# Kernel tuning notes

Hardware: AMD Instinct MI355X
Metric: run time of the kernel (lower is better)

The kernel has to match this reference:

```python
import jax, jax.numpy as jnp
import numpy as np

B, T, N, D, M, H, L, FF = 8, 128, 24, 128, 9, 8, 4, 1024
F = D // H          # spatial head dim = 16
HD = D // H         # temporal head dim = 16
ND = N * D          # 3072
NM = N * M          # 216


def setup_inputs() -> dict:
    key = jax.random.key(0)
    ks = jax.random.split(key, 24)
    w = lambda k, shape, s=0.05: (jax.random.normal(k, shape, jnp.float32) * s)
    z = lambda shape: jnp.zeros(shape, jnp.float32)
    return {
        "inputs": jax.random.normal(ks[0], (B, T, NM), jnp.float32),
        "emb_W": w(ks[1], (N, M, D)), "emb_b": z((N, D)),
        "sp_Wq": w(ks[2], (L, H, N, D, F)), "sp_bq": z((L, H, N, F)),
        "sp_Wk": w(ks[3], (L, H, D, F)), "sp_bk": z((L, H, F)),
        "sp_Wv": w(ks[4], (L, H, D, F)), "sp_bv": z((L, H, F)),
        "tmp_Win": w(ks[5], (L, N, 3 * D, D)), "tmp_bin": z((L, N, 3 * D)),
        "tmp_Wout": w(ks[6], (L, N, D, D)), "tmp_bout": z((L, N, D)),
        "ff_W1": w(ks[7], (L, ND, FF)), "ff_b1": z((L, FF)),
        "ff_W2": w(ks[8], (L, FF, ND)), "ff_b2": z((L, ND)),
        "ln_g": jnp.ones((L, ND), jnp.float32), "ln_b": z((L, ND)),
        "fin_W": w(ks[9], (ND, NM)), "fin_b": z((NM,)),
    }


def _ln(x, g, b):
    m = jnp.mean(x, -1, keepdims=True)
    v = jnp.mean(jnp.square(x - m), -1, keepdims=True)
    return (x - m) * jax.lax.rsqrt(v + 1e-5) * g + b


def _pos_encoding():
    # standard sinusoidal PE; original adds it over the FIRST axis of the
    # (B, T, N*D) tensor (applied before the permute), so index by B.
    pos = jnp.arange(B, dtype=jnp.float32)[:, None]
    div = jnp.exp(jnp.arange(0, ND, 2, dtype=jnp.float32) * (-np.log(10000.0) / ND))
    pe = jnp.zeros((B, ND), jnp.float32)
    pe = pe.at[:, 0::2].set(jnp.sin(pos * div)).at[:, 1::2].set(jnp.cos(pos * div))
    return pe


def reference(inputs, emb_W, emb_b, sp_Wq, sp_bq, sp_Wk, sp_bk, sp_Wv, sp_bv,
              tmp_Win, tmp_bin, tmp_Wout, tmp_bout, ff_W1, ff_b1, ff_W2, ff_b2,
              ln_g, ln_b, fin_W, fin_b):
    # joint embedding: (B,T,N,M) @ (N,M,D) -> (B,T,N,D)
    x4 = inputs.reshape(B, T, N, M)
    emb = (jnp.einsum('btnm,nmd->btnd', x4, emb_W) + emb_b).reshape(B, T, ND)
    emb = emb + _pos_encoding()[:, None, :]
    h = emb.transpose(1, 0, 2)                     # (T, B, ND)
    # PyTorch float attn_mask is ADDED to scores: +1.0 strictly below diagonal
    mask = jnp.tril(jnp.ones((T, T), jnp.float32), -1)
    for l in range(L):
        xr = h.reshape(T, B, N, D)
        # ---- spatial attention (shared K/V, per-joint Q, per head) ----
        k = jnp.einsum('tbnd,hdf->tbhnf', xr, sp_Wk[l]) + sp_bk[l][:, None, :]
        v = jnp.einsum('tbnd,hdf->tbhnf', xr, sp_Wv[l]) + sp_bv[l][:, None, :]
        q = jnp.einsum('tbnd,hndf->tbhnf', xr, sp_Wq[l]) + sp_bq[l]
        a = jax.nn.softmax(jnp.einsum('tbhnf,tbhmf->tbhnm', q, k) / jnp.sqrt(jnp.float32(F)), -1)
        sp = jnp.einsum('tbhnm,tbhmf->tbhnf', a, v)
        sp = sp.transpose(0, 1, 3, 2, 4).reshape(T, B, ND)   # joint-major, heads concat within joint
        sp = _ln(sp + h, ln_g[l], ln_b[l])
        # ---- temporal attention (per-joint nn.MultiheadAttention) ----
        Wq_t, Wk_t, Wv_t = tmp_Win[l, :, :D], tmp_Win[l, :, D:2 * D], tmp_Win[l, :, 2 * D:]
        bq_t, bk_t, bv_t = tmp_bin[l, :, :D], tmp_bin[l, :, D:2 * D], tmp_bin[l, :, 2 * D:]
        qt = (jnp.einsum('tbnd,ned->tbne', xr, Wq_t) + bq_t).reshape(T, B, N, H, HD)
        kt = (jnp.einsum('tbnd,ned->tbne', xr, Wk_t) + bk_t).reshape(T, B, N, H, HD)
        vt = (jnp.einsum('tbnd,ned->tbne', xr, Wv_t) + bv_t).reshape(T, B, N, H, HD)
        st = jnp.einsum('tbnhe,sbnhe->bnhts', qt, kt) / jnp.sqrt(jnp.float32(HD)) + mask
        at = jax.nn.softmax(st, -1)
        ot = jnp.einsum('bnhts,sbnhe->tbnhe', at, vt).reshape(T, B, N, D)
        tp = (jnp.einsum('tbnd,nod->tbno', ot, tmp_Wout[l]) + tmp_bout[l]).reshape(T, B, ND)
        tp = _ln(tp + h, ln_g[l], ln_b[l])
        # ---- FFN (no activation in original) + residual + shared LN ----
        a2 = sp + tp
        o = (a2 @ ff_W1[l] + ff_b1[l]) @ ff_W2[l] + ff_b2[l]
        h = _ln(o + a2, ln_g[l], ln_b[l])
    out = h @ fin_W + fin_b                        # (T, B, NM)
    return out.transpose(1, 0, 2) + inputs
```

## Files before the change

kernel.cpp:

```cpp
#include <hip/hip_runtime.h>
#include <hip/hip_bf16.h>
#include <math.h>

constexpr int kB = 8, kT = 128, kN = 24, kD = 128, kM = 9, kH = 8, kL = 4, kFF = 1024;
constexpr int kF = 16;
constexpr int kHD = 16;
constexpr int kND = kN * kD;
constexpr int kNM = kN * kM;
constexpr int kP = kB * kT;

using bf16x8 = __attribute__((ext_vector_type(8))) short;
using f32x4  = __attribute__((ext_vector_type(4))) float;
typedef __hip_bfloat16 bf16;

__device__ __forceinline__ void load_lds16(const void* g, void* l) {
  __builtin_amdgcn_global_load_lds(
      (const __attribute__((address_space(1))) void*)g,
      (__attribute__((address_space(3))) void*)l, 16, 0, 0);
}

template<int BM, int BN, bool OUTBF>
__global__ __launch_bounds__(256) void mfma_gemm(
    const bf16* __restrict__ A, const bf16* __restrict__ Bm,
    const float* __restrict__ bias, void* __restrict__ Cv,
    int M, int Nc, int K, int ldB, int sAi, int sCi,
    long offAg, long offBg, long offCg, int sBg)
{
  constexpr int WM = BM / 2, WN = BN / 2;
  constexpr int MT = WM / 16, NT = WN / 16;
  constexpr int ASLOTS = BM * 8;
  constexpr int BSLOTS = BN * 8;
  constexpr int CSTR = BN + 4;
  __shared__ __align__(16) char smem[(BM + BN) * 64 * 2];
  bf16* As = (bf16*)smem;
  bf16* Bs = (bf16*)(smem + BM * 64 * 2);
  float* Cs = (float*)smem;

  int g = blockIdx.z;
  A  += offAg * g;
  Bm += offBg * g;
  long cbase = offCg * (long)g;
  int bOff = sBg * g;

  int m0 = blockIdx.y * BM, n0 = blockIdx.x * BN;
  int tid = threadIdx.x, lane = tid & 63, wave = tid >> 6;
  int wm = wave >> 1, wn = wave & 1;
  int fr = lane & 15, fq = lane >> 4;

  f32x4 acc[MT][NT] = {};

  for (int kk = 0; kk < K; kk += 64) {
#pragma unroll
    for (int s = tid; s < ASLOTS; s += 256) {
      int m = s >> 3, kq = (s & 7) ^ (m & 7);
      load_lds16(A + (size_t)(m0 + m) * sAi + (kk + kq * 8), &As[s * 8]);
    }
#pragma unroll
    for (int s = tid; s < BSLOTS; s += 256) {
      int n = s >> 3, kq = (s & 7) ^ (n & 7);
      int nr = n0 + n; if (nr > Nc - 1) nr = Nc - 1;
      load_lds16(Bm + (size_t)nr * ldB + (kk + kq * 8), &Bs[s * 8]);
    }
    __syncthreads();
#pragma unroll
    for (int ks = 0; ks < 2; ks++) {
      bf16x8 af[MT], bfr[NT];
#pragma unroll
      for (int i = 0; i < MT; i++) {
        int row = wm * WM + i * 16 + fr;
        af[i] = *(const bf16x8*)&As[row * 64 + (((ks * 4 + fq) ^ (row & 7)) * 8)];
      }
#pragma unroll
      for (int j = 0; j < NT; j++) {
        int row = wn * WN + j * 16 + fr;
        bfr[j] = *(const bf16x8*)&Bs[row * 64 + (((ks * 4 + fq) ^ (row & 7)) * 8)];
      }
#pragma unroll
      for (int i = 0; i < MT; i++)
#pragma unroll
        for (int j = 0; j < NT; j++)
          acc[i][j] = __builtin_amdgcn_mfma_f32_16x16x32_bf16(af[i], bfr[j], acc[i][j], 0, 0, 0);
    }
    __syncthreads();
  }

  constexpr int NCHUNK = BN / 16;
  int tcol = tid & (NCHUNK - 1);
  int trow = tid / NCHUNK;
  int colbase = n0 + tcol * 16;
  float vb[16];
  if (trow < 32) {
#pragma unroll
    for (int jj = 0; jj < 16; jj++)
      vb[jj] = bias ? bias[bOff + colbase + jj] : 0.f;
  }
#pragma unroll
  for (int i = 0; i < MT; i++) {
    __syncthreads();
#pragma unroll
    for (int j = 0; j < NT; j++)
#pragma unroll
      for (int r = 0; r < 4; r++)
        Cs[(wm * 16 + fq * 4 + r) * CSTR + wn * WN + j * 16 + fr] = acc[i][j][r];
    __syncthreads();
    if (trow < 32) {
      int row = m0 + (trow >> 4) * WM + i * 16 + (trow & 15);
      float vals[16];
#pragma unroll
      for (int jj = 0; jj < 4; jj++)
        *(float4*)&vals[jj * 4] = *(const float4*)&Cs[trow * CSTR + tcol * 16 + jj * 4];
#pragma unroll
      for (int jj = 0; jj < 16; jj++) vals[jj] += vb[jj];
      if (OUTBF) {
        bf16* cp = (bf16*)Cv + cbase + (size_t)row * sCi + colbase;
        union { bf16 h[8]; uint4 v; } pk;
#pragma unroll
        for (int half = 0; half < 2; half++) {
          if (colbase + half * 8 + 8 <= Nc) {
#pragma unroll
            for (int jj = 0; jj < 8; jj++) pk.h[jj] = __float2bfloat16(vals[half * 8 + jj]);
            *(uint4*)(cp + half * 8) = pk.v;
          }
        }
      } else {
        float* cp = (float*)Cv + cbase + (size_t)row * sCi + colbase;
#pragma unroll
        for (int jj = 0; jj < 4; jj++)
          if (colbase + jj * 4 + 4 <= Nc) *(float4*)(cp + jj * 4) = *(float4*)&vals[jj * 4];
      }
    }
  }
}


__global__ __launch_bounds__(256) void trans_cvt_kernel(
    const float* __restrict__ in, bf16* __restrict__ out,
    int R, int C, long inStrideZ, long outStrideZ)
{
  __shared__ float t[64][65];
  int c0 = blockIdx.x * 64, r0 = blockIdx.y * 64;
  in  += inStrideZ  * blockIdx.z;
  out += outStrideZ * blockIdx.z;
  int tx = threadIdx.x & 63, ty = threadIdx.x >> 6;
  for (int rr = ty; rr < 64; rr += 4) {
    int r = r0 + rr, c = c0 + tx;
    t[rr][tx] = (r < R && c < C) ? in[(size_t)r * C + c] : 0.f;
  }
  __syncthreads();
  for (int cc = ty; cc < 64; cc += 4) {
    int c = c0 + cc, r = r0 + tx;
    if (c < C && r < R) out[(size_t)c * R + r] = __float2bfloat16(t[tx][cc]);
  }
}

__global__ __launch_bounds__(256) void cvt_kernel(
    const float* __restrict__ in, bf16* __restrict__ out, int n)
{
  int i = blockIdx.x * 256 + threadIdx.x;
  if (i < n) out[i] = __float2bfloat16(in[i]);
}

__global__ __launch_bounds__(256) void build_spW_kernel(
    const float* __restrict__ Wq, const float* __restrict__ Wk,
    const float* __restrict__ Wv, const float* __restrict__ Win,
    bf16* __restrict__ outW)
{
  int i = blockIdx.x * 256 + threadIdx.x;
  int d = i & 127;
  int rest = i >> 7;
  int r = rest % 768;
  int n = (rest / 768) % 24;
  int l = rest / (768 * 24);
  int hh = (r & 127) >> 4, f = r & 15;
  float v;
  if (r < 128)      v = Wq[((((size_t)l * kH + hh) * kN + n) * kD + d) * kF + f];
  else if (r < 256) v = Wk[(((size_t)l * kH + hh) * kD + d) * kF + f];
  else if (r < 384) v = Wv[(((size_t)l * kH + hh) * kD + d) * kF + f];
  else              v = Win[(((size_t)l * kN + n) * 384 + (r - 384)) * kD + d];
  outW[i] = __float2bfloat16(v);
}

__global__ __launch_bounds__(256) void build_spb_kernel(
    const float* __restrict__ bq, const float* __restrict__ bk,
    const float* __restrict__ bv, const float* __restrict__ bin,
    float* __restrict__ outb)
{
  int i = blockIdx.x * 256 + threadIdx.x;
  if (i >= kL * 24 * 768) return;
  int r = i % 768;
  int n = (i / 768) % 24;
  int l = i / (768 * 24);
  int hh = (r & 127) >> 4, f = r & 15;
  float v;
  if (r < 128)      v = bq[(((size_t)l * kH + hh) * kN + n) * kF + f];
  else if (r < 256) v = bk[((size_t)l * kH + hh) * kF + f];
  else if (r < 384) v = bv[((size_t)l * kH + hh) * kF + f];
  else              v = bin[((size_t)l * kN + n) * 384 + (r - 384)];
  outb[i] = v;
}

__global__ __launch_bounds__(256) void emb_kernel(
    const float* __restrict__ inp, const float* __restrict__ W,
    const float* __restrict__ bias, float* __restrict__ h, bf16* __restrict__ hbb)
{
  int p = blockIdx.x;
  int t = p / kB, b = p % kB;
  __shared__ float xs[kNM];
  for (int i = threadIdx.x; i < kNM; i += 256)
    xs[i] = inp[((size_t)b * kT + t) * kNM + i];
  __syncthreads();
  const float c1 = -logf(10000.f) / (float)kND;
  for (int c = threadIdx.x; c < kND; c += 256) {
    int n = c / kD, d = c % kD;
    float acc = bias[n * kD + d];
#pragma unroll
    for (int m = 0; m < kM; m++)
      acc += xs[n * kM + m] * W[(n * kM + m) * kD + d];
    float ang = (float)b * expf((float)(c & ~1) * c1);
    acc += (c & 1) ? cosf(ang) : sinf(ang);
    h[(size_t)p * kND + c] = acc;
    hbb[(size_t)p * kND + c] = __float2bfloat16(acc);
  }
}

__global__ __launch_bounds__(192) void sp_attn_kernel(
    const bf16* __restrict__ qkv, float* __restrict__ out)
{
  int p = blockIdx.x;
  __shared__ float s[24 * 388];
  for (int i = threadIdx.x; i < 2304; i += 192) {
    int n = i / 96, c4 = (i % 96) * 4;
    ushort4 u = *(const ushort4*)((const ushort*)qkv + ((size_t)n * kP + p) * 768 + c4);
    float4 f;
    f.x = __bfloat162float(*(const bf16*)&u.x);
    f.y = __bfloat162float(*(const bf16*)&u.y);
    f.z = __bfloat162float(*(const bf16*)&u.z);
    f.w = __bfloat162float(*(const bf16*)&u.w);
    *(float4*)&s[n * 388 + c4] = f;
  }
  __syncthreads();
  int hh = threadIdx.x / 24, n = threadIdx.x % 24;
  const float* qr = s + n * 388 + hh * 16;
  float sc[24];
  float mx = -1e30f;
#pragma unroll
  for (int m = 0; m < 24; m++) {
    const float* kr = s + m * 388 + 128 + hh * 16;
    float d = 0.f;
#pragma unroll
    for (int f = 0; f < 16; f++) d += qr[f] * kr[f];
    d *= 0.25f;
    sc[m] = d;
    mx = fmaxf(mx, d);
  }
  float sum = 0.f;
#pragma unroll
  for (int m = 0; m < 24; m++) { float e = __expf(sc[m] - mx); sc[m] = e; sum += e; }
  float inv = 1.f / sum;
  float* orow = out + (size_t)p * kND + n * kD + hh * 16;
#pragma unroll
  for (int f = 0; f < 16; f++) {
    float acc = 0.f;
#pragma unroll
    for (int m = 0; m < 24; m++) acc += sc[m] * s[m * 388 + 256 + hh * 16 + f];
    orow[f] = acc * inv;
  }
}

__global__ __launch_bounds__(128) void t_attn_mfma(
    const bf16* __restrict__ qkv, bf16* __restrict__ ot)
{
  int g = blockIdx.x;
  int hh = g & 7, n = (g >> 3) % 24, b = g / 192;
  __shared__ __align__(16) ushort Qs[128][40];
  __shared__ __align__(16) ushort Ks[128][40];
  __shared__ __align__(16) ushort Vt[16][136];
  __shared__ __align__(16) ushort Ps[128][136];

  for (int idx = threadIdx.x; idx < 512; idx += 128) {
    int t = idx >> 2, e4 = (idx & 3) * 4;
    const ushort* src = (const ushort*)qkv +
        ((size_t)n * kP + (size_t)t * kB + b) * 768 + 384 + hh * 16 + e4;
    ushort4 q4 = *(const ushort4*)(src);
    ushort4 k4 = *(const ushort4*)(src + 128);
    ushort4 v4 = *(const ushort4*)(src + 256);
    *(ushort4*)&Qs[t][e4] = q4;
    *(ushort4*)&Ks[t][e4] = k4;
    *(ushort4*)&Qs[t][16 + e4] = make_ushort4(0, 0, 0, 0);
    *(ushort4*)&Ks[t][16 + e4] = make_ushort4(0, 0, 0, 0);
    Vt[e4][t] = v4.x; Vt[e4 + 1][t] = v4.y; Vt[e4 + 2][t] = v4.z; Vt[e4 + 3][t] = v4.w;
  }
  __syncthreads();

  int lane = threadIdx.x & 63, w = threadIdx.x >> 6;
  int c = lane & 15, quad = lane >> 4;

  bf16x8 aq[4];
#pragma unroll
  for (int mt = 0; mt < 4; mt++)
    aq[mt] = *(const bf16x8*)&Qs[w * 64 + mt * 16 + c][quad * 8];
  f32x4 acc[4][8];
#pragma unroll
  for (int nt = 0; nt < 8; nt++) {
    bf16x8 bk = *(const bf16x8*)&Ks[nt * 16 + c][quad * 8];
#pragma unroll
    for (int mt = 0; mt < 4; mt++) {
      f32x4 z = {0.f, 0.f, 0.f, 0.f};
      acc[mt][nt] = __builtin_amdgcn_mfma_f32_16x16x32_bf16(aq[mt], bk, z, 0, 0, 0);
    }
  }

  f32x4 invv[4];
#pragma unroll
  for (int mt = 0; mt < 4; mt++) {
    int tbase = w * 64 + mt * 16 + quad * 4;
    f32x4 rm = {-1e30f, -1e30f, -1e30f, -1e30f};
#pragma unroll
    for (int nt = 0; nt < 8; nt++) {
      int s = nt * 16 + c;
#pragma unroll
      for (int r = 0; r < 4; r++) {
        float x = acc[mt][nt][r] * 0.25f + ((s < tbase + r) ? 1.f : 0.f);
        acc[mt][nt][r] = x;
        rm[r] = fmaxf(rm[r], x);
      }
    }
#pragma unroll
    for (int off = 1; off < 16; off <<= 1)
#pragma unroll
      for (int r = 0; r < 4; r++) rm[r] = fmaxf(rm[r], __shfl_xor(rm[r], off, 64));
    f32x4 rs = {0.f, 0.f, 0.f, 0.f};
#pragma unroll
    for (int nt = 0; nt < 8; nt++)
#pragma unroll
      for (int r = 0; r < 4; r++) {
        float pp = __expf(acc[mt][nt][r] - rm[r]);
        acc[mt][nt][r] = pp;
        rs[r] += pp;
      }
#pragma unroll
    for (int off = 1; off < 16; off <<= 1)
#pragma unroll
      for (int r = 0; r < 4; r++) rs[r] += __shfl_xor(rs[r], off, 64);
#pragma unroll
    for (int r = 0; r < 4; r++) invv[mt][r] = 1.f / rs[r];
#pragma unroll
    for (int nt = 0; nt < 8; nt++)
#pragma unroll
      for (int r = 0; r < 4; r++) {
        bf16 pb = __float2bfloat16(acc[mt][nt][r]);
        Ps[tbase + r][nt * 16 + c] = *(ushort*)&pb;
      }
  }

  f32x4 o[4] = {};
#pragma unroll
  for (int ks = 0; ks < 128; ks += 32) {
    bf16x8 bv = *(const bf16x8*)&Vt[c][ks + quad * 8];
#pragma unroll
    for (int mt = 0; mt < 4; mt++) {
      bf16x8 ap = *(const bf16x8*)&Ps[w * 64 + mt * 16 + c][ks + quad * 8];
      o[mt] = __builtin_amdgcn_mfma_f32_16x16x32_bf16(ap, bv, o[mt], 0, 0, 0);
    }
  }

#pragma unroll
  for (int mt = 0; mt < 4; mt++) {
#pragma unroll
    for (int r = 0; r < 4; r++) {
      int t = w * 64 + mt * 16 + quad * 4 + r;
      float val = o[mt][r] * invv[mt][r];
      ot[((size_t)n * kP + (size_t)t * kB + b) * 128 + hh * 16 + c] = __float2bfloat16(val);
    }
  }
}

__global__ __launch_bounds__(256) void fuse_a2_kernel(
    const float* __restrict__ sp, const float* __restrict__ tp,
    const float* __restrict__ h, const float* __restrict__ g,
    const float* __restrict__ be, float* __restrict__ a2, bf16* __restrict__ a2b)
{
  int row = blockIdx.x;
  const float* s1p = sp + (size_t)row * kND;
  const float* s2p = tp + (size_t)row * kND;
  const float* hp  = h  + (size_t)row * kND;
  float x1[12], x2[12];
  float sum1 = 0.f, sum2 = 0.f;
#pragma unroll
  for (int i = 0; i < 12; i++) {
    int c = threadIdx.x + 256 * i;
    float hv = hp[c];
    x1[i] = s1p[c] + hv; x2[i] = s2p[c] + hv;
    sum1 += x1[i]; sum2 += x2[i];
  }
  __shared__ float red1[4], red2[4];
#pragma unroll
  for (int o = 32; o > 0; o >>= 1) { sum1 += __shfl_down(sum1, o, 64); sum2 += __shfl_down(sum2, o, 64); }
  int wid = threadIdx.x >> 6;
  if ((threadIdx.x & 63) == 0) { red1[wid] = sum1; red2[wid] = sum2; }
  __syncthreads();
  float mean1 = (red1[0] + red1[1] + red1[2] + red1[3]) * (1.f / kND);
  float mean2 = (red2[0] + red2[1] + red2[2] + red2[3]) * (1.f / kND);
  __syncthreads();
  float v1 = 0.f, v2 = 0.f;
#pragma unroll
  for (int i = 0; i < 12; i++) {
    float d1 = x1[i] - mean1, d2 = x2[i] - mean2;
    v1 += d1 * d1; v2 += d2 * d2;
  }
#pragma unroll
  for (int o = 32; o > 0; o >>= 1) { v1 += __shfl_down(v1, o, 64); v2 += __shfl_down(v2, o, 64); }
  if ((threadIdx.x & 63) == 0) { red1[wid] = v1; red2[wid] = v2; }
  __syncthreads();
  float r1 = rsqrtf((red1[0] + red1[1] + red1[2] + red1[3]) * (1.f / kND) + 1e-5f);
  float r2 = rsqrtf((red2[0] + red2[1] + red2[2] + red2[3]) * (1.f / kND) + 1e-5f);
#pragma unroll
  for (int i = 0; i < 12; i++) {
    int c = threadIdx.x + 256 * i;
    float gc = g[c], bc = be[c];
    float o = (x1[i] - mean1) * r1 * gc + bc + (x2[i] - mean2) * r2 * gc + bc;
    a2[(size_t)row * kND + c] = o;
    a2b[(size_t)row * kND + c] = __float2bfloat16(o);
  }
}

__global__ __launch_bounds__(256) void add_ln_dual_kernel(
    const float* __restrict__ a, const float* __restrict__ b,
    const float* __restrict__ g, const float* __restrict__ be,
    float* __restrict__ out, bf16* __restrict__ outb)
{
  int row = blockIdx.x;
  const float* ar = a + (size_t)row * kND;
  const float* br = b + (size_t)row * kND;
  float v[12];
  float s = 0.f;
#pragma unroll
  for (int i = 0; i < 12; i++) {
    int c = threadIdx.x + 256 * i;
    float x = ar[c] + br[c];
    v[i] = x; s += x;
  }
  __shared__ float red[4];
#pragma unroll
  for (int o = 32; o > 0; o >>= 1) s += __shfl_down(s, o, 64);
  int wid = threadIdx.x >> 6;
  if ((threadIdx.x & 63) == 0) red[wid] = s;
  __syncthreads();
  float mean = (red[0] + red[1] + red[2] + red[3]) * (1.f / kND);
  __syncthreads();
  float vs = 0.f;
#pragma unroll
  for (int i = 0; i < 12; i++) { float d = v[i] - mean; vs += d * d; }
#pragma unroll
  for (int o = 32; o > 0; o >>= 1) vs += __shfl_down(vs, o, 64);
  if ((threadIdx.x & 63) == 0) red[wid] = vs;
  __syncthreads();
  float rstd = rsqrtf((red[0] + red[1] + red[2] + red[3]) * (1.f / kND) + 1e-5f);
#pragma unroll
  for (int i = 0; i < 12; i++) {
    int c = threadIdx.x + 256 * i;
    float o = (v[i] - mean) * rstd * g[c] + be[c];
    out[(size_t)row * kND + c] = o;
    outb[(size_t)row * kND + c] = __float2bfloat16(o);
  }
}

__global__ __launch_bounds__(256) void ff1_reduce_kernel(
    const float* __restrict__ part, const float* __restrict__ bias,
    bf16* __restrict__ out)
{
  int i4 = (blockIdx.x * 256 + threadIdx.x) * 4;
  const size_t S = (size_t)kP * kFF;
  float4 p0 = *(const float4*)(part + i4);
  float4 p1 = *(const float4*)(part + S + i4);
  float4 p2 = *(const float4*)(part + 2 * S + i4);
  int col = i4 & (kFF - 1);
#pragma unroll
  for (int j = 0; j < 4; j++) {
    float v = ((const float*)&p0)[j] + ((const float*)&p1)[j] + ((const float*)&p2)[j]
            + bias[col + j];
    out[i4 + j] = __float2bfloat16(v);
  }
}

__global__ __launch_bounds__(256) void final_reduce_add_kernel(
    const float* __restrict__ part, const float* __restrict__ fin_b,
    const float* __restrict__ inp, float* __restrict__ out)
{
  int i = blockIdx.x * 256 + threadIdx.x;
  if (i >= kB * kT * kNM) return;
  int c = i % kNM;
  int rem = i / kNM;
  int t = rem % kT, b = rem / kT;
  size_t pi = (size_t)(t * kB + b) * kNM + c;
  const size_t S = (size_t)kP * kNM;
  float v = fin_b[c] + inp[i];
#pragma unroll
  for (int z = 0; z < 8; z++) v += part[z * S + pi];
  out[i] = v;
}

extern "C" void kernel_launch(void* const* d_in, const int* in_sizes, int n_in,
                              void* d_out, int out_size, void* d_ws, size_t ws_size,
                              hipStream_t stream)
{
  const float* inputs   = (const float*)d_in[0];
  const float* emb_W    = (const float*)d_in[1];
  const float* emb_b    = (const float*)d_in[2];
  const float* sp_Wq    = (const float*)d_in[3];
  const float* sp_bq    = (const float*)d_in[4];
  const float* sp_Wk    = (const float*)d_in[5];
  const float* sp_bk    = (const float*)d_in[6];
  const float* sp_Wv    = (const float*)d_in[7];
  const float* sp_bv    = (const float*)d_in[8];
  const float* tmp_Win  = (const float*)d_in[9];
  const float* tmp_bin  = (const float*)d_in[10];
  const float* tmp_Wout = (const float*)d_in[11];
  const float* tmp_bout = (const float*)d_in[12];
  const float* ff_W1    = (const float*)d_in[13];
  const float* ff_b1    = (const float*)d_in[14];
  const float* ff_W2    = (const float*)d_in[15];
  const float* ff_b2    = (const float*)d_in[16];
  const float* ln_g     = (const float*)d_in[17];
  const float* ln_b     = (const float*)d_in[18];
  const float* fin_W    = (const float*)d_in[19];
  const float* fin_b    = (const float*)d_in[20];
  float* out = (float*)d_out;

  char* wp = (char*)d_ws;
  size_t off = 0;
  auto alloc = [&](size_t bytes) { void* p = wp + off; off += (bytes + 255) & ~(size_t)255; return p; };
  bf16* spW   = (bf16*)alloc((size_t)kL * 24 * 768 * 128 * 2);
  bf16* toWb  = (bf16*)alloc((size_t)kL * 24 * 128 * 128 * 2);
  bf16* W1t   = (bf16*)alloc((size_t)kL * kFF * kND * 2);
  bf16* W2t   = (bf16*)alloc((size_t)kL * kND * kFF * 2);
  bf16* finWt = (bf16*)alloc((size_t)kNM * kND * 2);
  float* spbc = (float*)alloc((size_t)kL * 24 * 768 * 4);
  float* hb   = (float*)alloc((size_t)kP * kND * 4);
  bf16*  hbb  = (bf16*) alloc((size_t)kP * kND * 2);
  bf16*  qkvb = (bf16*) alloc((size_t)24 * kP * 768 * 2);
  float* sp   = (float*)alloc((size_t)kP * kND * 4);
  float* tp   = (float*)alloc((size_t)kP * kND * 4);
  float* a2   = (float*)alloc((size_t)kP * kND * 4);
  bf16*  a2b  = (bf16*) alloc((size_t)kP * kND * 2);
  bf16*  f1b  = (bf16*) alloc((size_t)kP * kFF * 2);
  bf16*  otb  = (bf16*) alloc((size_t)24 * kP * 128 * 2);
  float* ffpart  = sp;
  float* finpart = tp;

  trans_cvt_kernel<<<dim3(kFF / 64, kND / 64, kL), 256, 0, stream>>>(
      ff_W1, W1t, kND, kFF, (long)kND * kFF, (long)kFF * kND);
  trans_cvt_kernel<<<dim3(kND / 64, kFF / 64, kL), 256, 0, stream>>>(
      ff_W2, W2t, kFF, kND, (long)kFF * kND, (long)kND * kFF);
  trans_cvt_kernel<<<dim3((kNM + 63) / 64, kND / 64, 1), 256, 0, stream>>>(
      fin_W, finWt, kND, kNM, 0L, 0L);
  cvt_kernel<<<(kL * 24 * 128 * 128 + 255) / 256, 256, 0, stream>>>(
      tmp_Wout, toWb, kL * 24 * 128 * 128);
  build_spW_kernel<<<(kL * 24 * 768 * 128) / 256, 256, 0, stream>>>(
      sp_Wq, sp_Wk, sp_Wv, tmp_Win, spW);
  build_spb_kernel<<<(kL * 24 * 768 + 255) / 256, 256, 0, stream>>>(
      sp_bq, sp_bk, sp_bv, tmp_bin, spbc);

  emb_kernel<<<kP, 256, 0, stream>>>(inputs, emb_W, emb_b, hb, hbb);

  for (int l = 0; l < kL; l++) {
    const float* lg = ln_g + (size_t)l * kND;
    const float* lb = ln_b + (size_t)l * kND;

    mfma_gemm<128, 128, true><<<dim3(6, 8, 24), 256, 0, stream>>>(
        hbb, spW + (size_t)l * 24 * 768 * 128, spbc + (size_t)l * 24 * 768, qkvb,
        kP, 768, 128, 128, kND, 768,
        128, 768 * 128, (long)kP * 768, 768);

    sp_attn_kernel<<<kP, 192, 0, stream>>>(qkvb, sp);
    t_attn_mfma<<<kB * 24 * 8, 128, 0, stream>>>(qkvb, otb);

    mfma_gemm<64, 64, false><<<dim3(2, 16, 24), 256, 0, stream>>>(
        otb, toWb + (size_t)l * 24 * 128 * 128, tmp_bout + (size_t)l * 24 * 128, tp,
        kP, 128, 128, 128, 128, kND,
        (long)kP * 128, 128 * 128, 128, 128);

    fuse_a2_kernel<<<kP, 256, 0, stream>>>(sp, tp, hb, lg, lb, a2, a2b);

    mfma_gemm<64, 64, false><<<dim3(kFF / 64, kP / 64, 3), 256, 0, stream>>>(
        a2b, W1t + (size_t)l * kFF * kND, nullptr, ffpart,
        kP, kFF, kND / 3, kND, kND, kFF,
        kND / 3, kND / 3, (long)kP * kFF, 0);
    ff1_reduce_kernel<<<(kP * kFF / 4) / 256, 256, 0, stream>>>(
        ffpart, ff_b1 + (size_t)l * kFF, f1b);

    mfma_gemm<64, 64, false><<<dim3(kND / 64, kP / 64, 1), 256, 0, stream>>>(
        f1b, W2t + (size_t)l * kND * kFF, ff_b2 + (size_t)l * kND, tp,
        kP, kND, kFF, kFF, kFF, kND, 0, 0, 0, 0);

    add_ln_dual_kernel<<<kP, 256, 0, stream>>>(tp, a2, lg, lb, hb, hbb);
  }

  mfma_gemm<64, 64, false><<<dim3((kNM + 63) / 64, kP / 64, 8), 256, 0, stream>>>(
      hbb, finWt, nullptr, finpart,
      kP, kNM, kND / 8, kND, kND, kNM,
      kND / 8, kND / 8, (long)kP * kNM, 0);
  final_reduce_add_kernel<<<(kB * kT * kNM + 255) / 256, 256, 0, stream>>>(
      finpart, fin_b, inputs, out);
}
```

Baseline: 862.5 us.

## Vectorize memory accesses across conversion, embedding, attention and layernorm kernels

Rewrites many elementwise and memory-bound kernels to use 128-bit and 64-bit vector loads and stores: the weight transpose/convert, the flat convert, the spatial weight build, the embedding, the spatial attention inner loops, the temporal attention staging, both layernorm kernels and the FF1 reduction. The aim is fewer memory instructions and better coalescing in these bandwidth-bound kernels. The transpose now assumes row and column tails are aligned, and the convert kernel drops any remainder that is not a multiple of eight elements.

```diff
diff --git a/kernel.cpp b/kernel.cpp
--- a/kernel.cpp
+++ b/kernel.cpp
@@ -141,23 +141,46 @@
   int c0 = blockIdx.x * 64, r0 = blockIdx.y * 64;
   in  += inStrideZ  * blockIdx.z;
   out += outStrideZ * blockIdx.z;
-  int tx = threadIdx.x & 63, ty = threadIdx.x >> 6;
-  for (int rr = ty; rr < 64; rr += 4) {
-    int r = r0 + rr, c = c0 + tx;
-    t[rr][tx] = (r < R && c < C) ? in[(size_t)r * C + c] : 0.f;
-  }
-  __syncthreads();
-  for (int cc = ty; cc < 64; cc += 4) {
-    int c = c0 + cc, r = r0 + tx;
-    if (c < C && r < R) out[(size_t)c * R + r] = __float2bfloat16(t[tx][cc]);
+  int tid = threadIdx.x;
+  for (int s = tid; s < 1024; s += 256) {
+    int rr = s >> 4, c4 = (s & 15) * 4;
+    int r = r0 + rr, c = c0 + c4;
+    float4 v;
+    if (c + 4 <= C) v = *(const float4*)&in[(size_t)r * C + c];
+    else {
+      float tmp[4];
+#pragma unroll
+      for (int j = 0; j < 4; j++) tmp[j] = (c + j < C) ? in[(size_t)r * C + c + j] : 0.f;
+      v = *(float4*)tmp;
+    }
+    *(float4*)&t[rr][c4] = v;
+  }
+  __syncthreads();
+  for (int s = tid; s < 512; s += 256) {
+    int cc = s >> 3, r8 = (s & 7) * 8;
+    int c = c0 + cc;
+    if (c < C) {
+      union { bf16 h[8]; uint4 v; } pk;
+#pragma unroll
+      for (int j = 0; j < 8; j++) pk.h[j] = __float2bfloat16(t[r8 + j][cc]);
+      *(uint4*)&out[(size_t)c * R + r0 + r8] = pk.v;
+    }
   }
 }
 
 __global__ __launch_bounds__(256) void cvt_kernel(
     const float* __restrict__ in, bf16* __restrict__ out, int n)
 {
-  int i = blockIdx.x * 256 + threadIdx.x;
-  if (i < n) out[i] = __float2bfloat16(in[i]);
+  int i8 = (blockIdx.x * 256 + threadIdx.x) * 8;
+  if (i8 + 8 > n) return;
+  float4 v0 = *(const float4*)(in + i8);
+  float4 v1 = *(const float4*)(in + i8 + 4);
+  union { bf16 h[8]; uint4 v; } pk;
+  pk.h[0] = __float2bfloat16(v0.x); pk.h[1] = __float2bfloat16(v0.y);
+  pk.h[2] = __float2bfloat16(v0.z); pk.h[3] = __float2bfloat16(v0.w);
+  pk.h[4] = __float2bfloat16(v1.x); pk.h[5] = __float2bfloat16(v1.y);
+  pk.h[6] = __float2bfloat16(v1.z); pk.h[7] = __float2bfloat16(v1.w);
+  *(uint4*)(out + i8) = pk.v;
 }
 
 __global__ __launch_bounds__(256) void build_spW_kernel(
@@ -165,19 +188,30 @@
     const float* __restrict__ Wv, const float* __restrict__ Win,
     bf16* __restrict__ outW)
 {
-  int i = blockIdx.x * 256 + threadIdx.x;
-  int d = i & 127;
-  int rest = i >> 7;
+  int i8 = (blockIdx.x * 256 + threadIdx.x) * 8;
+  int d = i8 & 127;
+  int rest = i8 >> 7;
   int r = rest % 768;
   int n = (rest / 768) % 24;
   int l = rest / (768 * 24);
   int hh = (r & 127) >> 4, f = r & 15;
-  float v;
-  if (r < 128)      v = Wq[((((size_t)l * kH + hh) * kN + n) * kD + d) * kF + f];
-  else if (r < 256) v = Wk[(((size_t)l * kH + hh) * kD + d) * kF + f];
-  else if (r < 384) v = Wv[(((size_t)l * kH + hh) * kD + d) * kF + f];
-  else              v = Win[(((size_t)l * kN + n) * 384 + (r - 384)) * kD + d];
-  outW[i] = __float2bfloat16(v);
+  union { bf16 h[8]; uint4 v; } pk;
+  if (r >= 384) {
+    const float* src = &Win[((((size_t)l * kN + n) * 384) + (r - 384)) * kD + d];
+    float4 v0 = *(const float4*)src, v1 = *(const float4*)(src + 4);
+    pk.h[0] = __float2bfloat16(v0.x); pk.h[1] = __float2bfloat16(v0.y);
+    pk.h[2] = __float2bfloat16(v0.z); pk.h[3] = __float2bfloat16(v0.w);
+    pk.h[4] = __float2bfloat16(v1.x); pk.h[5] = __float2bfloat16(v1.y);
+    pk.h[6] = __float2bfloat16(v1.z); pk.h[7] = __float2bfloat16(v1.w);
+  } else {
+    const float* base;
+    if (r < 128)      base = &Wq[((((size_t)l * kH + hh) * kN + n) * kD + d) * kF + f];
+    else if (r < 256) base = &Wk[(((size_t)l * kH + hh) * kD + d) * kF + f];
+    else              base = &Wv[(((size_t)l * kH + hh) * kD + d) * kF + f];
+#pragma unroll
+    for (int j = 0; j < 8; j++) pk.h[j] = __float2bfloat16(base[(size_t)j * kF]);
+  }
+  *(uint4*)&outW[i8] = pk.v;
 }
 
 __global__ __launch_bounds__(256) void build_spb_kernel(
@@ -206,20 +240,29 @@
   int p = blockIdx.x;
   int t = p / kB, b = p % kB;
   __shared__ float xs[kNM];
-  for (int i = threadIdx.x; i < kNM; i += 256)
-    xs[i] = inp[((size_t)b * kT + t) * kNM + i];
+  if (threadIdx.x < kNM)
+    xs[threadIdx.x] = inp[((size_t)b * kT + t) * kNM + threadIdx.x];
   __syncthreads();
   const float c1 = -logf(10000.f) / (float)kND;
-  for (int c = threadIdx.x; c < kND; c += 256) {
-    int n = c / kD, d = c % kD;
-    float acc = bias[n * kD + d];
-#pragma unroll
-    for (int m = 0; m < kM; m++)
-      acc += xs[n * kM + m] * W[(n * kM + m) * kD + d];
-    float ang = (float)b * expf((float)(c & ~1) * c1);
-    acc += (c & 1) ? cosf(ang) : sinf(ang);
-    h[(size_t)p * kND + c] = acc;
-    hbb[(size_t)p * kND + c] = __float2bfloat16(acc);
+  for (int c4 = threadIdx.x; c4 < kND / 4; c4 += 256) {
+    int c = c4 * 4;
+    int n = c >> 7, d = c & 127;
+    float4 acc = *(const float4*)&bias[n * kD + d];
+#pragma unroll
+    for (int m = 0; m < kM; m++) {
+      float xv = xs[n * kM + m];
+      float4 w = *(const float4*)&W[((size_t)(n * kM + m)) * kD + d];
+      acc.x += xv * w.x; acc.y += xv * w.y; acc.z += xv * w.z; acc.w += xv * w.w;
+    }
+    float ang0 = (float)b * expf((float)c * c1);
+    float ang1 = (float)b * expf((float)(c + 2) * c1);
+    acc.x += sinf(ang0); acc.y += cosf(ang0);
+    acc.z += sinf(ang1); acc.w += cosf(ang1);
+    *(float4*)&h[(size_t)p * kND + c] = acc;
+    union { bf16 h4[4]; uint2 v; } pk;
+    pk.h4[0] = __float2bfloat16(acc.x); pk.h4[1] = __float2bfloat16(acc.y);
+    pk.h4[2] = __float2bfloat16(acc.z); pk.h4[3] = __float2bfloat16(acc.w);
+    *(uint2*)&hbb[(size_t)p * kND + c] = pk.v;
   }
 }
 
@@ -240,15 +283,18 @@
   }
   __syncthreads();
   int hh = threadIdx.x / 24, n = threadIdx.x % 24;
-  const float* qr = s + n * 388 + hh * 16;
+  const float4* qr = (const float4*)(s + n * 388 + hh * 16);
+  float4 q0 = qr[0], q1 = qr[1], q2 = qr[2], q3 = qr[3];
   float sc[24];
   float mx = -1e30f;
 #pragma unroll
   for (int m = 0; m < 24; m++) {
-    const float* kr = s + m * 388 + 128 + hh * 16;
-    float d = 0.f;
-#pragma unroll
-    for (int f = 0; f < 16; f++) d += qr[f] * kr[f];
+    const float4* kr = (const float4*)(s + m * 388 + 128 + hh * 16);
+    float4 k0 = kr[0], k1 = kr[1], k2 = kr[2], k3 = kr[3];
+    float d = q0.x * k0.x + q0.y * k0.y + q0.z * k0.z + q0.w * k0.w
+            + q1.x * k1.x + q1.y * k1.y + q1.z * k1.z + q1.w * k1.w
+            + q2.x * k2.x + q2.y * k2.y + q2.z * k2.z + q2.w * k2.w
+            + q3.x * k3.x + q3.y * k3.y + q3.z * k3.z + q3.w * k3.w;
     d *= 0.25f;
     sc[m] = d;
     mx = fmaxf(mx, d);
@@ -257,14 +303,26 @@
 #pragma unroll
   for (int m = 0; m < 24; m++) { float e = __expf(sc[m] - mx); sc[m] = e; sum += e; }
   float inv = 1.f / sum;
+  float4 o0 = {0,0,0,0}, o1 = {0,0,0,0}, o2 = {0,0,0,0}, o3 = {0,0,0,0};
+#pragma unroll
+  for (int m = 0; m < 24; m++) {
+    const float4* vr = (const float4*)(s + m * 388 + 256 + hh * 16);
+    float4 v0 = vr[0], v1 = vr[1], v2 = vr[2], v3 = vr[3];
+    float w = sc[m];
+    o0.x += w * v0.x; o0.y += w * v0.y; o0.z += w * v0.z; o0.w += w * v0.w;
+    o1.x += w * v1.x; o1.y += w * v1.y; o1.z += w * v1.z; o1.w += w * v1.w;
+    o2.x += w * v2.x; o2.y += w * v2.y; o2.z += w * v2.z; o2.w += w * v2.w;
+    o3.x += w * v3.x; o3.y += w * v3.y; o3.z += w * v3.z; o3.w += w * v3.w;
+  }
   float* orow = out + (size_t)p * kND + n * kD + hh * 16;
-#pragma unroll
-  for (int f = 0; f < 16; f++) {
-    float acc = 0.f;
-#pragma unroll
-    for (int m = 0; m < 24; m++) acc += sc[m] * s[m * 388 + 256 + hh * 16 + f];
-    orow[f] = acc * inv;
-  }
+  o0.x *= inv; o0.y *= inv; o0.z *= inv; o0.w *= inv;
+  o1.x *= inv; o1.y *= inv; o1.z *= inv; o1.w *= inv;
+  o2.x *= inv; o2.y *= inv; o2.z *= inv; o2.w *= inv;
+  o3.x *= inv; o3.y *= inv; o3.z *= inv; o3.w *= inv;
+  *(float4*)(orow)      = o0;
+  *(float4*)(orow + 4)  = o1;
+  *(float4*)(orow + 8)  = o2;
+  *(float4*)(orow + 12) = o3;
 }
 
 __global__ __launch_bounds__(128) void t_attn_mfma(
@@ -277,18 +335,20 @@
   __shared__ __align__(16) ushort Vt[16][136];
   __shared__ __align__(16) ushort Ps[128][136];
 
-  for (int idx = threadIdx.x; idx < 512; idx += 128) {
-    int t = idx >> 2, e4 = (idx & 3) * 4;
+  for (int idx = threadIdx.x; idx < 256; idx += 128) {
+    int t = idx >> 1, e8 = (idx & 1) * 8;
     const ushort* src = (const ushort*)qkv +
-        ((size_t)n * kP + (size_t)t * kB + b) * 768 + 384 + hh * 16 + e4;
-    ushort4 q4 = *(const ushort4*)(src);
-    ushort4 k4 = *(const ushort4*)(src + 128);
-    ushort4 v4 = *(const ushort4*)(src + 256);
-    *(ushort4*)&Qs[t][e4] = q4;
-    *(ushort4*)&Ks[t][e4] = k4;
-    *(ushort4*)&Qs[t][16 + e4] = make_ushort4(0, 0, 0, 0);
-    *(ushort4*)&Ks[t][16 + e4] = make_ushort4(0, 0, 0, 0);
-    Vt[e4][t] = v4.x; Vt[e4 + 1][t] = v4.y; Vt[e4 + 2][t] = v4.z; Vt[e4 + 3][t] = v4.w;
+        ((size_t)n * kP + (size_t)t * kB + b) * 768 + 384 + hh * 16 + e8;
+    uint4 q = *(const uint4*)(src);
+    uint4 k = *(const uint4*)(src + 128);
+    uint4 v = *(const uint4*)(src + 256);
+    *(uint4*)&Qs[t][e8] = q;
+    *(uint4*)&Ks[t][e8] = k;
+    *(uint4*)&Qs[t][16 + e8] = make_uint4(0, 0, 0, 0);
+    *(uint4*)&Ks[t][16 + e8] = make_uint4(0, 0, 0, 0);
+    const ushort* vp = (const ushort*)&v;
+#pragma unroll
+    for (int j = 0; j < 8; j++) Vt[e8 + j][t] = vp[j];
   }
   __syncthreads();
 
@@ -381,17 +441,20 @@
     const float* __restrict__ be, float* __restrict__ a2, bf16* __restrict__ a2b)
 {
   int row = blockIdx.x;
-  const float* s1p = sp + (size_t)row * kND;
-  const float* s2p = tp + (size_t)row * kND;
-  const float* hp  = h  + (size_t)row * kND;
-  float x1[12], x2[12];
+  const float4* s1p = (const float4*)(sp + (size_t)row * kND);
+  const float4* s2p = (const float4*)(tp + (size_t)row * kND);
+  const float4* hp  = (const float4*)(h  + (size_t)row * kND);
+  float4 x1[3], x2[3];
   float sum1 = 0.f, sum2 = 0.f;
 #pragma unroll
-  for (int i = 0; i < 12; i++) {
+  for (int i = 0; i < 3; i++) {
     int c = threadIdx.x + 256 * i;
-    float hv = hp[c];
-    x1[i] = s1p[c] + hv; x2[i] = s2p[c] + hv;
-    sum1 += x1[i]; sum2 += x2[i];
+    float4 hv = hp[c], a = s1p[c], bb = s2p[c];
+    a.x += hv.x; a.y += hv.y; a.z += hv.z; a.w += hv.w;
+    bb.x += hv.x; bb.y += hv.y; bb.z += hv.z; bb.w += hv.w;
+    x1[i] = a; x2[i] = bb;
+    sum1 += a.x + a.y + a.z + a.w;
+    sum2 += bb.x + bb.y + bb.z + bb.w;
   }
   __shared__ float red1[4], red2[4];
 #pragma unroll
@@ -404,9 +467,12 @@
   __syncthreads();
   float v1 = 0.f, v2 = 0.f;
 #pragma unroll
-  for (int i = 0; i < 12; i++) {
-    float d1 = x1[i] - mean1, d2 = x2[i] - mean2;
-    v1 += d1 * d1; v2 += d2 * d2;
+  for (int i = 0; i < 3; i++) {
+    float4 a = x1[i], bb = x2[i];
+    v1 += (a.x - mean1) * (a.x - mean1) + (a.y - mean1) * (a.y - mean1)
+        + (a.z - mean1) * (a.z - mean1) + (a.w - mean1) * (a.w - mean1);
+    v2 += (bb.x - mean2) * (bb.x - mean2) + (bb.y - mean2) * (bb.y - mean2)
+        + (bb.z - mean2) * (bb.z - mean2) + (bb.w - mean2) * (bb.w - mean2);
   }
 #pragma unroll
   for (int o = 32; o > 0; o >>= 1) { v1 += __shfl_down(v1, o, 64); v2 += __shfl_down(v2, o, 64); }
@@ -414,13 +480,22 @@
   __syncthreads();
   float r1 = rsqrtf((red1[0] + red1[1] + red1[2] + red1[3]) * (1.f / kND) + 1e-5f);
   float r2 = rsqrtf((red2[0] + red2[1] + red2[2] + red2[3]) * (1.f / kND) + 1e-5f);
-#pragma unroll
-  for (int i = 0; i < 12; i++) {
+  const float4* g4 = (const float4*)g;
+  const float4* b4 = (const float4*)be;
+#pragma unroll
+  for (int i = 0; i < 3; i++) {
     int c = threadIdx.x + 256 * i;
-    float gc = g[c], bc = be[c];
-    float o = (x1[i] - mean1) * r1 * gc + bc + (x2[i] - mean2) * r2 * gc + bc;
-    a2[(size_t)row * kND + c] = o;
-    a2b[(size_t)row * kND + c] = __float2bfloat16(o);
+    float4 gc = g4[c], bc = b4[c];
+    float4 a = x1[i], bb = x2[i], o;
+    o.x = (a.x - mean1) * r1 * gc.x + bc.x + (bb.x - mean2) * r2 * gc.x + bc.x;
+    o.y = (a.y - mean1) * r1 * gc.y + bc.y + (bb.y - mean2) * r2 * gc.y + bc.y;
+    o.z = (a.z - mean1) * r1 * gc.z + bc.z + (bb.z - mean2) * r2 * gc.z + bc.z;
+    o.w = (a.w - mean1) * r1 * gc.w + bc.w + (bb.w - mean2) * r2 * gc.w + bc.w;
+    *(float4*)(a2 + (size_t)row * kND + c * 4) = o;
+    union { bf16 h4[4]; uint2 v; } pk;
+    pk.h4[0] = __float2bfloat16(o.x); pk.h4[1] = __float2bfloat16(o.y);
+    pk.h4[2] = __float2bfloat16(o.z); pk.h4[3] = __float2bfloat16(o.w);
+    *(uint2*)(a2b + (size_t)row * kND + c * 4) = pk.v;
   }
 }
 
@@ -430,15 +505,17 @@
     float* __restrict__ out, bf16* __restrict__ outb)
 {
   int row = blockIdx.x;
-  const float* ar = a + (size_t)row * kND;
-  const float* br = b + (size_t)row * kND;
-  float v[12];
+  const float4* ar = (const float4*)(a + (size_t)row * kND);
+  const float4* br = (const float4*)(b + (size_t)row * kND);
+  float4 v[3];
   float s = 0.f;
 #pragma unroll
-  for (int i = 0; i < 12; i++) {
+  for (int i = 0; i < 3; i++) {
     int c = threadIdx.x + 256 * i;
-    float x = ar[c] + br[c];
-    v[i] = x; s += x;
+    float4 x = ar[c], y = br[c];
+    x.x += y.x; x.y += y.y; x.z += y.z; x.w += y.w;
+    v[i] = x;
+    s += x.x + x.y + x.z + x.w;
   }
   __shared__ float red[4];
 #pragma unroll
@@ -450,18 +527,31 @@
   __syncthreads();
   float vs = 0.f;
 #pragma unroll
-  for (int i = 0; i < 12; i++) { float d = v[i] - mean; vs += d * d; }
+  for (int i = 0; i < 3; i++) {
+    float4 x = v[i];
+    vs += (x.x - mean) * (x.x - mean) + (x.y - mean) * (x.y - mean)
+        + (x.z - mean) * (x.z - mean) + (x.w - mean) * (x.w - mean);
+  }
 #pragma unroll
   for (int o = 32; o > 0; o >>= 1) vs += __shfl_down(vs, o, 64);
   if ((threadIdx.x & 63) == 0) red[wid] = vs;
   __syncthreads();
   float rstd = rsqrtf((red[0] + red[1] + red[2] + red[3]) * (1.f / kND) + 1e-5f);
-#pragma unroll
-  for (int i = 0; i < 12; i++) {
+  const float4* g4 = (const float4*)g;
+  const float4* b4 = (const float4*)be;
+#pragma unroll
+  for (int i = 0; i < 3; i++) {
     int c = threadIdx.x + 256 * i;
-    float o = (v[i] - mean) * rstd * g[c] + be[c];
-    out[(size_t)row * kND + c] = o;
-    outb[(size_t)row * kND + c] = __float2bfloat16(o);
+    float4 gc = g4[c], bc = b4[c], x = v[i], o;
+    o.x = (x.x - mean) * rstd * gc.x + bc.x;
+    o.y = (x.y - mean) * rstd * gc.y + bc.y;
+    o.z = (x.z - mean) * rstd * gc.z + bc.z;
+    o.w = (x.w - mean) * rstd * gc.w + bc.w;
+    *(float4*)(out + (size_t)row * kND + c * 4) = o;
+    union { bf16 h4[4]; uint2 v2; } pk;
+    pk.h4[0] = __float2bfloat16(o.x); pk.h4[1] = __float2bfloat16(o.y);
+    pk.h4[2] = __float2bfloat16(o.z); pk.h4[3] = __float2bfloat16(o.w);
+    *(uint2*)(outb + (size_t)row * kND + c * 4) = pk.v2;
   }
 }
 
@@ -475,12 +565,13 @@
   float4 p1 = *(const float4*)(part + S + i4);
   float4 p2 = *(const float4*)(part + 2 * S + i4);
   int col = i4 & (kFF - 1);
-#pragma unroll
-  for (int j = 0; j < 4; j++) {
-    float v = ((const float*)&p0)[j] + ((const float*)&p1)[j] + ((const float*)&p2)[j]
-            + bias[col + j];
-    out[i4 + j] = __float2bfloat16(v);
-  }
+  float4 bb = *(const float4*)(bias + col);
+  union { bf16 h4[4]; uint2 v; } pk;
+  pk.h4[0] = __float2bfloat16(p0.x + p1.x + p2.x + bb.x);
+  pk.h4[1] = __float2bfloat16(p0.y + p1.y + p2.y + bb.y);
+  pk.h4[2] = __float2bfloat16(p0.z + p1.z + p2.z + bb.z);
+  pk.h4[3] = __float2bfloat16(p0.w + p1.w + p2.w + bb.w);
+  *(uint2*)(out + i4) = pk.v;
 }
 
 __global__ __launch_bounds__(256) void final_reduce_add_kernel(
@@ -554,9 +645,9 @@
       ff_W2, W2t, kFF, kND, (long)kFF * kND, (long)kND * kFF);
   trans_cvt_kernel<<<dim3((kNM + 63) / 64, kND / 64, 1), 256, 0, stream>>>(
       fin_W, finWt, kND, kNM, 0L, 0L);
-  cvt_kernel<<<(kL * 24 * 128 * 128 + 255) / 256, 256, 0, stream>>>(
+  cvt_kernel<<<(kL * 24 * 128 * 128 / 8) / 256, 256, 0, stream>>>(
       tmp_Wout, toWb, kL * 24 * 128 * 128);
-  build_spW_kernel<<<(kL * 24 * 768 * 128) / 256, 256, 0, stream>>>(
+  build_spW_kernel<<<(kL * 24 * 768 * 128 / 8) / 256, 256, 0, stream>>>(
       sp_Wq, sp_Wk, sp_Wv, tmp_Win, spW);
   build_spb_kernel<<<(kL * 24 * 768 + 255) / 256, 256, 0, stream>>>(
       sp_bq, sp_bk, sp_bv, tmp_bin, spbc);
```

Result: faster. 799.4 us (-7.3%).
